# Kernel optimization log

Measured on AMD Instinct MI355X. Metric: run time of the kernel, lower is better.

## Reference

```python
import jax, jax.numpy as jnp
import numpy as np

NUM_ITERS = 5
MIN_SCALE = 0.5
MAX_SCALE = 2.0
EPS = 1e-8


def setup_inputs() -> dict:
    key = jax.random.key(0)
    k1, k2 = jax.random.split(key)
    B, N, M = 16, 4096, 4096
    source = jax.random.normal(k1, (B, N, 3), dtype=jnp.float32)
    target = jax.random.normal(k2, (B, M, 3), dtype=jnp.float32)
    return {"source": source, "target": target}


def _sq_cdist(a, b):
    # squared euclidean distance matrix (B,N,M) via quadratic expansion
    a2 = jnp.sum(a * a, axis=-1)[:, :, None]
    b2 = jnp.sum(b * b, axis=-1)[:, None, :]
    ab = jnp.einsum('bnd,bmd->bnm', a, b)
    return jnp.maximum(a2 + b2 - 2.0 * ab, 0.0)


def _umeyama(source, target_corr):
    # optimal similarity transform (R, t, scale), Umeyama
    B = source.shape[0]
    mu_src = jnp.mean(source, axis=1, keepdims=True)       # (B,1,3)
    mu_tgt = jnp.mean(target_corr, axis=1, keepdims=True)  # (B,1,3)
    src_c = source - mu_src
    tgt_c = target_corr - mu_tgt
    H = jnp.einsum('bnd,bne->bde', src_c, tgt_c)           # (B,3,3)
    U, S, Vh = jnp.linalg.svd(H)
    V = jnp.swapaxes(Vh, 1, 2)
    det_UV = jnp.linalg.det(jnp.einsum('bij,bkj->bik', V, U))  # det(V U^T)
    d_diag = jnp.concatenate(
        [jnp.ones((B, 2), dtype=source.dtype), det_UV[:, None]], axis=1)  # (B,3)
    # R = V @ diag(d) @ U^T
    R = jnp.einsum('bij,bj,bkj->bik', V, d_diag, U)
    var_src = jnp.sum(src_c * src_c, axis=(1, 2))          # (B,)
    trace_S = jnp.sum(S * d_diag, axis=1)                  # (B,)
    scale = (trace_S / (var_src + EPS))[:, None, None]
    scale = jnp.clip(scale, MIN_SCALE, MAX_SCALE)
    t = mu_tgt - scale * jnp.einsum('bnd,bed->bne', mu_src, R)
    return R, t, scale


def reference(source, target):
    # ICP iterations (no-grad in original -> stop_gradient on final transform)
    src_current = source
    for _ in range(NUM_ITERS):
        dist = _sq_cdist(src_current, target)              # (B,N,M)
        min_idx = jnp.argmin(dist, axis=2)                 # (B,N)
        tgt_corr = jnp.take_along_axis(target, min_idx[:, :, None], axis=1)
        R, t, scale = _umeyama(source, tgt_corr)
        src_current = scale * jnp.einsum('bnd,bed->bne', source, R) + t
    R = jax.lax.stop_gradient(R)
    t = jax.lax.stop_gradient(t)
    scale = jax.lax.stop_gradient(scale)
    aligned_source = scale * jnp.einsum('bnd,bed->bne', source, R) + t
    final_dist = _sq_cdist(aligned_source, target)
    min_src2tgt = jnp.min(final_dist, axis=2)
    min_tgt2src = jnp.min(final_dist, axis=1)
    chamfer = jnp.mean(min_src2tgt, axis=1) + jnp.mean(min_tgt2src, axis=1)
    return jnp.mean(chamfer), aligned_source
```

## Files before the change

kernel.cpp:

```cpp
#include <hip/hip_runtime.h>
#include <math.h>

#define BLOCK 256
#define NB    16
#define NN_   4096
#define MM_   4096
#define NITER 5
#define P     4
#define SCH   4
#define KCH   32
#define TCH   128
#define KCHF  16
#define TCHF  256
#define B2    1024

#define OFF_STATS 0
#define OFF_T     64
#define OFF_CH    320
#define OFF_ND    2048
#define OFF_FA    67584
#define OFF_FB    133120
#define CLR_BASE  2048
#define CLR_CNT   196608

typedef __attribute__((ext_vector_type(2))) float f32x2;

__device__ __forceinline__ f32x2 pk_fma(f32x2 a, f32x2 b, f32x2 c) {
#if defined(__has_builtin) && __has_builtin(__builtin_elementwise_fma)
  return __builtin_elementwise_fma(a, b, c);
#else
  return a * b + c;
#endif
}

__device__ __forceinline__ void atomic_min_f(float* p, float v) {
  atomicMin((unsigned int*)p, __float_as_uint(v));
}

__global__ __launch_bounds__(BLOCK) void icp_init(const float* __restrict__ src,
                                                  float* __restrict__ ws) {
  int b = blockIdx.x, tid = threadIdx.x;
  for (int i = b*BLOCK + tid; i < CLR_CNT; i += NB*BLOCK)
    ws[CLR_BASE + i] = INFINITY;
  const float* sb = src + (size_t)b * NN_ * 3;
  float sx = 0.f, sy = 0.f, sz = 0.f, ss = 0.f;
  for (int n = tid; n < NN_; n += BLOCK) {
    float x = sb[3*n], y = sb[3*n+1], z = sb[3*n+2];
    sx += x; sy += y; sz += z;
    ss += fmaf(x, x, fmaf(y, y, z*z));
  }
  __shared__ float red[16];
  for (int m = 32; m; m >>= 1) {
    sx += __shfl_xor(sx, m); sy += __shfl_xor(sy, m);
    sz += __shfl_xor(sz, m); ss += __shfl_xor(ss, m);
  }
  int wave = tid >> 6;
  if ((tid & 63) == 0) {
    red[wave*4+0] = sx; red[wave*4+1] = sy; red[wave*4+2] = sz; red[wave*4+3] = ss;
  }
  __syncthreads();
  if (tid == 0) {
    for (int w = 1; w < 4; ++w) {
      sx += red[w*4+0]; sy += red[w*4+1]; sz += red[w*4+2]; ss += red[w*4+3];
    }
    float* st = ws + OFF_STATS + b*4;
    st[0] = sx; st[1] = sy; st[2] = sz; st[3] = ss;
    float* T = ws + OFF_T + b*16;
    T[0]=1.f; T[1]=0.f; T[2]=0.f;
    T[3]=0.f; T[4]=1.f; T[5]=0.f;
    T[6]=0.f; T[7]=0.f; T[8]=1.f;
    T[9]=0.f; T[10]=0.f; T[11]=0.f; T[12]=1.f;
  }
}

__global__ __launch_bounds__(BLOCK, 8) void icp_nn1(const float* __restrict__ src,
                                                    const float* __restrict__ tgt,
                                                    float* __restrict__ ws) {
  __shared__ __align__(16) float tx_[TCH], ty_[TCH], tz_[TCH], tw_[TCH];
  int b = blockIdx.z, kc = blockIdx.y, tid = threadIdx.x;
  int n0 = blockIdx.x * (BLOCK * P) + tid;
  const float* T = ws + OFF_T + b*16;
  float sc = T[12];
  f32x2 nxp[P], nyp[P], nzp[P], p2p[P];
#pragma unroll
  for (int k = 0; k < P; ++k) {
    const float* sp = src + ((size_t)b * NN_ + n0 + k*BLOCK) * 3;
    float sx = sp[0], sy = sp[1], sz = sp[2];
    float px = fmaf(sc, fmaf(T[0], sx, fmaf(T[1], sy, T[2]*sz)), T[9]);
    float py = fmaf(sc, fmaf(T[3], sx, fmaf(T[4], sy, T[5]*sz)), T[10]);
    float pz = fmaf(sc, fmaf(T[6], sx, fmaf(T[7], sy, T[8]*sz)), T[11]);
    nxp[k].x = nxp[k].y = -2.f*px;
    nyp[k].x = nyp[k].y = -2.f*py;
    nzp[k].x = nzp[k].y = -2.f*pz;
    float p2 = fmaf(px, px, fmaf(py, py, pz*pz));
    p2p[k].x = p2p[k].y = p2;
  }
  if (tid < TCH) {
    int j = tid;
    const float* tp = tgt + ((size_t)b * MM_ + kc * TCH + j) * 3;
    float tx = tp[0], ty = tp[1], tz = tp[2];
    tx_[j] = tx; ty_[j] = ty; tz_[j] = tz;
    tw_[j] = fmaf(tx, tx, fmaf(ty, ty, tz*tz));
  }
  __syncthreads();

  int jbase = kc * TCH;
  float best[P];
#pragma unroll
  for (int k = 0; k < P; ++k) best[k] = INFINITY;
#pragma unroll 4
  for (int j = 0; j < TCH; j += 2) {
    f32x2 TX = *(const f32x2*)&tx_[j];
    f32x2 TY = *(const f32x2*)&ty_[j];
    f32x2 TZ = *(const f32x2*)&tz_[j];
    f32x2 TW = *(const f32x2*)&tw_[j];
    unsigned i0 = (unsigned)(jbase + j), i1 = i0 + 1;
#pragma unroll
    for (int k = 0; k < P; ++k) {
      f32x2 v = pk_fma(nxp[k], TX, pk_fma(nyp[k], TY, pk_fma(nzp[k], TZ, TW + p2p[k])));
      float p0 = __uint_as_float((__float_as_uint(v.x) & 0xFFFFF000u) | i0);
      float p1 = __uint_as_float((__float_as_uint(v.y) & 0xFFFFF000u) | i1);
      best[k] = fminf(fminf(p0, p1), best[k]);
    }
  }
#pragma unroll
  for (int k = 0; k < P; ++k)
    atomic_min_f(ws + OFF_ND + (size_t)b*NN_ + n0 + k*BLOCK, best[k]);
}

__global__ __launch_bounds__(B2) void icp_nn2u(const float* __restrict__ src,
                                               const float* __restrict__ tgt,
                                               float* __restrict__ ws) {
  __shared__ float red[16*12];
  __shared__ float sums[12];
  int b = blockIdx.x, tid = threadIdx.x;
  float acc[12];
#pragma unroll
  for (int c = 0; c < 12; ++c) acc[c] = 0.f;
  for (int g = 0; g < NN_/B2; ++g) {
    int n = g*B2 + tid;
    size_t slot = OFF_ND + (size_t)b*NN_ + n;
    float bd = ws[slot];
    ws[slot] = INFINITY;
    int bi = (int)(__float_as_uint(bd) & 4095u);
    const float* tp = tgt + ((size_t)b * MM_ + bi) * 3;
    const float* sp = src + ((size_t)b * NN_ + n) * 3;
    float tx = tp[0], ty = tp[1], tz = tp[2];
    float sx = sp[0], sy = sp[1], sz = sp[2];
    acc[0] += tx; acc[1] += ty; acc[2] += tz;
    acc[3] += sx*tx; acc[4] += sx*ty; acc[5] += sx*tz;
    acc[6] += sy*tx; acc[7] += sy*ty; acc[8] += sy*tz;
    acc[9] += sz*tx; acc[10] += sz*ty; acc[11] += sz*tz;
  }
#pragma unroll
  for (int c = 0; c < 12; ++c)
    for (int m = 32; m; m >>= 1) acc[c] += __shfl_xor(acc[c], m);
  int wave = tid >> 6;
  if ((tid & 63) == 0) {
#pragma unroll
    for (int c = 0; c < 12; ++c) red[wave*12 + c] = acc[c];
  }
  __syncthreads();
  if (tid < 12) {
    float s = 0.f;
    for (int w = 0; w < 16; ++w) s += red[w*12 + tid];
    sums[tid] = s;
  }
  __syncthreads();
  if (tid != 0) return;

  const float* st = ws + OFF_STATS + b*4;
  const float N = (float)NN_;
  float mus[3] = {st[0]/N, st[1]/N, st[2]/N};
  float var_src = st[3] - N*(mus[0]*mus[0] + mus[1]*mus[1] + mus[2]*mus[2]);
  float mut[3] = {sums[0]/N, sums[1]/N, sums[2]/N};
  float H[3][3];
  for (int d = 0; d < 3; ++d)
    for (int e = 0; e < 3; ++e)
      H[d][e] = sums[3 + 3*d + e] - N*mus[d]*mut[e];

  float A[3][3];
  for (int i = 0; i < 3; ++i)
    for (int j = 0; j < 3; ++j)
      A[i][j] = H[0][i]*H[0][j] + H[1][i]*H[1][j] + H[2][i]*H[2][j];
  float V[3][3] = {{1,0,0},{0,1,0},{0,0,1}};
  const int PP[3] = {0,0,1}, QQ[3] = {1,2,2};
  for (int sweep = 0; sweep < 7; ++sweep) {
    for (int r = 0; r < 3; ++r) {
      int p = PP[r], q = QQ[r];
      float apq = A[p][q];
      if (fabsf(apq) < 1e-30f) continue;
      float tau = (A[q][q] - A[p][p]) / (2.f*apq);
      float tt = (tau >= 0.f ? 1.f : -1.f) / (fabsf(tau) + sqrtf(1.f + tau*tau));
      float c = rsqrtf(1.f + tt*tt), s = tt*c;
      for (int k = 0; k < 3; ++k) { float akp=A[k][p], akq=A[k][q];
        A[k][p]=c*akp - s*akq; A[k][q]=s*akp + c*akq; }
      for (int k = 0; k < 3; ++k) { float apk=A[p][k], aqk=A[q][k];
        A[p][k]=c*apk - s*aqk; A[q][k]=s*apk + c*aqk; }
      for (int k = 0; k < 3; ++k) { float vkp=V[k][p], vkq=V[k][q];
        V[k][p]=c*vkp - s*vkq; V[k][q]=s*vkp + c*vkq; }
    }
  }
  float lam[3] = {A[0][0], A[1][1], A[2][2]};
  int o[3] = {0,1,2};
  if (lam[o[1]] > lam[o[0]]) { int t_=o[0]; o[0]=o[1]; o[1]=t_; }
  if (lam[o[2]] > lam[o[0]]) { int t_=o[0]; o[0]=o[2]; o[2]=t_; }
  if (lam[o[2]] > lam[o[1]]) { int t_=o[1]; o[1]=o[2]; o[2]=t_; }
  float v0[3] = {V[0][o[0]], V[1][o[0]], V[2][o[0]]};
  float v1[3] = {V[0][o[1]], V[1][o[1]], V[2][o[1]]};
  float v2[3] = {V[0][o[2]], V[1][o[2]], V[2][o[2]]};

  float hv0[3], hv1[3], hv2[3];
  for (int d = 0; d < 3; ++d) {
    hv0[d] = H[d][0]*v0[0] + H[d][1]*v0[1] + H[d][2]*v0[2];
    hv1[d] = H[d][0]*v1[0] + H[d][1]*v1[1] + H[d][2]*v1[2];
    hv2[d] = H[d][0]*v2[0] + H[d][1]*v2[1] + H[d][2]*v2[2];
  }
  float S0 = sqrtf(hv0[0]*hv0[0] + hv0[1]*hv0[1] + hv0[2]*hv0[2]);
  float u0[3];
  float inv0 = (S0 > 1e-20f) ? 1.f/S0 : 0.f;
  u0[0]=hv0[0]*inv0; u0[1]=hv0[1]*inv0; u0[2]=hv0[2]*inv0;
  if (S0 <= 1e-20f) { u0[0]=1.f; u0[1]=0.f; u0[2]=0.f; }
  float S1 = sqrtf(hv1[0]*hv1[0] + hv1[1]*hv1[1] + hv1[2]*hv1[2]);
  float d01 = u0[0]*hv1[0] + u0[1]*hv1[1] + u0[2]*hv1[2];
  float w1[3] = {hv1[0]-d01*u0[0], hv1[1]-d01*u0[1], hv1[2]-d01*u0[2]};
  float n1 = sqrtf(w1[0]*w1[0] + w1[1]*w1[1] + w1[2]*w1[2]);
  float u1[3];
  if (n1 > 1e-20f) { u1[0]=w1[0]/n1; u1[1]=w1[1]/n1; u1[2]=w1[2]/n1; }
  else {
    float ax = fabsf(u0[0]);
    float t0[3] = { ax < 0.9f ? 1.f : 0.f, ax < 0.9f ? 0.f : 1.f, 0.f };
    u1[0] = u0[1]*t0[2]-u0[2]*t0[1];
    u1[1] = u0[2]*t0[0]-u0[0]*t0[2];
    u1[2] = u0[0]*t0[1]-u0[1]*t0[0];
    float nn = sqrtf(u1[0]*u1[0]+u1[1]*u1[1]+u1[2]*u1[2]);
    u1[0]/=nn; u1[1]/=nn; u1[2]/=nn;
  }
  float u2[3] = {u0[1]*u1[2]-u0[2]*u1[1],
                 u0[2]*u1[0]-u0[0]*u1[2],
                 u0[0]*u1[1]-u0[1]*u1[0]};
  float s2p = u2[0]*hv2[0] + u2[1]*hv2[1] + u2[2]*hv2[2];
  float dV = v0[0]*(v1[1]*v2[2]-v1[2]*v2[1])
           - v0[1]*(v1[0]*v2[2]-v1[2]*v2[0])
           + v0[2]*(v1[0]*v2[1]-v1[1]*v2[0]);
  dV = (dV >= 0.f) ? 1.f : -1.f;
  float traceS = S0 + S1 + dV * s2p;

  float R[3][3];
  for (int i = 0; i < 3; ++i)
    for (int k = 0; k < 3; ++k)
      R[i][k] = v0[i]*u0[k] + v1[i]*u1[k] + dV*v2[i]*u2[k];

  float scale = traceS / (var_src + 1e-8f);
  scale = fminf(fmaxf(scale, 0.5f), 2.0f);
  float tv[3];
  for (int e = 0; e < 3; ++e)
    tv[e] = mut[e] - scale*(R[e][0]*mus[0] + R[e][1]*mus[1] + R[e][2]*mus[2]);

  float* T = ws + OFF_T + b*16;
  for (int e = 0; e < 3; ++e)
    for (int d = 0; d < 3; ++d)
      T[3*e + d] = R[e][d];
  T[9]  = tv[0]; T[10] = tv[1]; T[11] = tv[2];
  T[12] = scale;
}

__global__ __launch_bounds__(BLOCK, 8) void icp_final(const float* __restrict__ src,
                                                      const float* __restrict__ tgt,
                                                      float* __restrict__ out,
                                                      float* __restrict__ ws) {
  __shared__ __align__(16) float tx_[TCHF], ty_[TCHF], tz_[TCHF], tw_[TCHF];
  int b = blockIdx.z, yk = blockIdx.y, tid = threadIdx.x;
  int dir = yk >> 4, kc = yk & 15;
  const float* T = ws + OFF_T + b*16;
  float sc = T[12];
  int n0 = blockIdx.x * (BLOCK * P) + tid;
  f32x2 nxp[P], nyp[P], nzp[P];
  float pp[P];

  if (dir == 0) {
#pragma unroll
    for (int k = 0; k < P; ++k) {
      const float* sp = src + ((size_t)b * NN_ + n0 + k*BLOCK) * 3;
      float sx = sp[0], sy = sp[1], sz = sp[2];
      float px = fmaf(sc, fmaf(T[0], sx, fmaf(T[1], sy, T[2]*sz)), T[9]);
      float py = fmaf(sc, fmaf(T[3], sx, fmaf(T[4], sy, T[5]*sz)), T[10]);
      float pz = fmaf(sc, fmaf(T[6], sx, fmaf(T[7], sy, T[8]*sz)), T[11]);
      if (kc == 0) {
        float* op = out + 1 + ((size_t)b * NN_ + n0 + k*BLOCK) * 3;
        op[0] = px; op[1] = py; op[2] = pz;
      }
      pp[k] = fmaf(px, px, fmaf(py, py, pz*pz));
      nxp[k].x = nxp[k].y = -2.f*px;
      nyp[k].x = nyp[k].y = -2.f*py;
      nzp[k].x = nzp[k].y = -2.f*pz;
    }
    const float* tb = tgt + ((size_t)b * MM_ + kc * TCHF) * 3;
    {
      int j = tid;
      float tx = tb[3*j], ty = tb[3*j+1], tz = tb[3*j+2];
      tx_[j] = tx; ty_[j] = ty; tz_[j] = tz;
      tw_[j] = fmaf(tx, tx, fmaf(ty, ty, tz*tz));
    }
  } else {
#pragma unroll
    for (int k = 0; k < P; ++k) {
      const float* qp = tgt + ((size_t)b * MM_ + n0 + k*BLOCK) * 3;
      float qx = qp[0], qy = qp[1], qz = qp[2];
      pp[k] = fmaf(qx, qx, fmaf(qy, qy, qz*qz));
      nxp[k].x = nxp[k].y = -2.f*qx;
      nyp[k].x = nyp[k].y = -2.f*qy;
      nzp[k].x = nzp[k].y = -2.f*qz;
    }
    const float* sb = src + ((size_t)b * NN_ + kc * TCHF) * 3;
    {
      int j = tid;
      float sx = sb[3*j], sy = sb[3*j+1], sz = sb[3*j+2];
      float ax = fmaf(sc, fmaf(T[0], sx, fmaf(T[1], sy, T[2]*sz)), T[9]);
      float ay = fmaf(sc, fmaf(T[3], sx, fmaf(T[4], sy, T[5]*sz)), T[10]);
      float az = fmaf(sc, fmaf(T[6], sx, fmaf(T[7], sy, T[8]*sz)), T[11]);
      tx_[j] = ax; ty_[j] = ay; tz_[j] = az;
      tw_[j] = fmaf(ax, ax, fmaf(ay, ay, az*az));
    }
  }
  __syncthreads();

  float best[P];
#pragma unroll
  for (int k = 0; k < P; ++k) best[k] = INFINITY;
#pragma unroll 4
  for (int j = 0; j < TCHF; j += 2) {
    f32x2 TX = *(const f32x2*)&tx_[j];
    f32x2 TY = *(const f32x2*)&ty_[j];
    f32x2 TZ = *(const f32x2*)&tz_[j];
    f32x2 TW = *(const f32x2*)&tw_[j];
#pragma unroll
    for (int k = 0; k < P; ++k) {
      f32x2 v = pk_fma(nxp[k], TX, pk_fma(nyp[k], TY, pk_fma(nzp[k], TZ, TW)));
      best[k] = fminf(fminf(v.x, v.y), best[k]);
    }
  }
  float* dst = ws + (dir ? OFF_FB : OFF_FA);
#pragma unroll
  for (int k = 0; k < P; ++k) {
    float v = fmaxf(best[k] + pp[k], 0.f);
    atomic_min_f(dst + (size_t)b*NN_ + n0 + k*BLOCK, v);
  }
}

__global__ __launch_bounds__(BLOCK) void icp_fcomb(float* __restrict__ ws) {
  __shared__ float red[4*2];
  int b = blockIdx.x, tid = threadIdx.x;
  float sa = 0.f, sb = 0.f;
  for (int g = 0; g < NN_/BLOCK; ++g) {
    int n = g*BLOCK + tid;
    sa += ws[OFF_FA + (size_t)b*NN_ + n];
    sb += ws[OFF_FB + (size_t)b*NN_ + n];
  }
  for (int m = 32; m; m >>= 1) {
    sa += __shfl_xor(sa, m); sb += __shfl_xor(sb, m);
  }
  int wave = tid >> 6;
  if ((tid & 63) == 0) { red[wave*2] = sa; red[wave*2+1] = sb; }
  __syncthreads();
  if (tid == 0) {
    sa = red[0] + red[2] + red[4] + red[6];
    sb = red[1] + red[3] + red[5] + red[7];
    ws[OFF_CH + b] = sa / (float)NN_ + sb / (float)MM_;
  }
}

__global__ __launch_bounds__(64) void icp_finalize(float* __restrict__ out,
                                                   const float* __restrict__ ws) {
  if (threadIdx.x == 0) {
    float s = 0.f;
    for (int b = 0; b < NB; ++b) s += ws[OFF_CH + b];
    out[0] = s / (float)NB;
  }
}

extern "C" void kernel_launch(void* const* d_in, const int* in_sizes, int n_in,
                              void* d_out, int out_size, void* d_ws, size_t ws_size,
                              hipStream_t stream) {
  const float* src = (const float*)d_in[0];
  const float* tgt = (const float*)d_in[1];
  float* out = (float*)d_out;
  float* ws  = (float*)d_ws;

  icp_init<<<NB, BLOCK, 0, stream>>>(src, ws);
  for (int it = 0; it < NITER; ++it) {
    icp_nn1<<<dim3(SCH, KCH, NB), BLOCK, 0, stream>>>(src, tgt, ws);
    icp_nn2u<<<NB, B2, 0, stream>>>(src, tgt, ws);
  }
  icp_final<<<dim3(SCH, 2*KCHF, NB), BLOCK, 0, stream>>>(src, tgt, out, ws);
  icp_fcomb<<<NB, BLOCK, 0, stream>>>(ws);
  icp_finalize<<<1, 64, 0, stream>>>(out, ws);
}
```

Measured before the change: 304.8 us.

## Fuse Umeyama update and chamfer reduction into last-block tails via atomic counters

Removes the separate icp_nn2u, icp_fcomb and icp_finalize launches. Each per-batch reduction now runs in whichever block of the preceding nearest-neighbour kernel finishes last, detected with a threadfence plus an atomic counter. This cuts kernel launches from 14 to 7 and the launch gaps between them. In exchange, the correspondence gather and SVD run on 256 threads instead of 1024, serialising on one block per batch, and the reads and resets go through atomics.

```diff
diff --git a/kernel.cpp b/kernel.cpp
--- a/kernel.cpp
+++ b/kernel.cpp
@@ -12,11 +12,13 @@
 #define TCH   128
 #define KCHF  16
 #define TCHF  256
-#define B2    1024
 
 #define OFF_STATS 0
 #define OFF_T     64
 #define OFF_CH    320
+#define OFF_CNT   1024
+#define OFF_CNTF  1040
+#define OFF_CNTG  1056
 #define OFF_ND    2048
 #define OFF_FA    67584
 #define OFF_FB    133120
@@ -36,12 +38,20 @@
 __device__ __forceinline__ void atomic_min_f(float* p, float v) {
   atomicMin((unsigned int*)p, __float_as_uint(v));
 }
+__device__ __forceinline__ float atomic_ld_f(float* p) {
+  return __uint_as_float(atomicAdd((unsigned int*)p, 0u));
+}
+__device__ __forceinline__ void atomic_st_f(float* p, float v) {
+  atomicExch((unsigned int*)p, __float_as_uint(v));
+}
 
 __global__ __launch_bounds__(BLOCK) void icp_init(const float* __restrict__ src,
                                                   float* __restrict__ ws) {
   int b = blockIdx.x, tid = threadIdx.x;
   for (int i = b*BLOCK + tid; i < CLR_CNT; i += NB*BLOCK)
     ws[CLR_BASE + i] = INFINITY;
+  if (b == 0 && tid < 64)
+    ((unsigned*)(ws + OFF_CNT))[tid] = 0u;
   const float* sb = src + (size_t)b * NN_ * 3;
   float sx = 0.f, sy = 0.f, sz = 0.f, ss = 0.f;
   for (int n = tid; n < NN_; n += BLOCK) {
@@ -77,71 +87,79 @@
                                                     const float* __restrict__ tgt,
                                                     float* __restrict__ ws) {
   __shared__ __align__(16) float tx_[TCH], ty_[TCH], tz_[TCH], tw_[TCH];
+  __shared__ float redA[4*12];
+  __shared__ float sums[12];
+  __shared__ int lastFlag;
   int b = blockIdx.z, kc = blockIdx.y, tid = threadIdx.x;
   int n0 = blockIdx.x * (BLOCK * P) + tid;
-  const float* T = ws + OFF_T + b*16;
-  float sc = T[12];
-  f32x2 nxp[P], nyp[P], nzp[P], p2p[P];
-#pragma unroll
-  for (int k = 0; k < P; ++k) {
-    const float* sp = src + ((size_t)b * NN_ + n0 + k*BLOCK) * 3;
-    float sx = sp[0], sy = sp[1], sz = sp[2];
-    float px = fmaf(sc, fmaf(T[0], sx, fmaf(T[1], sy, T[2]*sz)), T[9]);
-    float py = fmaf(sc, fmaf(T[3], sx, fmaf(T[4], sy, T[5]*sz)), T[10]);
-    float pz = fmaf(sc, fmaf(T[6], sx, fmaf(T[7], sy, T[8]*sz)), T[11]);
-    nxp[k].x = nxp[k].y = -2.f*px;
-    nyp[k].x = nyp[k].y = -2.f*py;
-    nzp[k].x = nzp[k].y = -2.f*pz;
-    float p2 = fmaf(px, px, fmaf(py, py, pz*pz));
-    p2p[k].x = p2p[k].y = p2;
-  }
-  if (tid < TCH) {
-    int j = tid;
-    const float* tp = tgt + ((size_t)b * MM_ + kc * TCH + j) * 3;
-    float tx = tp[0], ty = tp[1], tz = tp[2];
-    tx_[j] = tx; ty_[j] = ty; tz_[j] = tz;
-    tw_[j] = fmaf(tx, tx, fmaf(ty, ty, tz*tz));
-  }
-  __syncthreads();
-
-  int jbase = kc * TCH;
-  float best[P];
-#pragma unroll
-  for (int k = 0; k < P; ++k) best[k] = INFINITY;
+  {
+    const float* T = ws + OFF_T + b*16;
+    float sc = T[12];
+    f32x2 nxp[P], nyp[P], nzp[P], p2p[P];
+#pragma unroll
+    for (int k = 0; k < P; ++k) {
+      const float* sp = src + ((size_t)b * NN_ + n0 + k*BLOCK) * 3;
+      float sx = sp[0], sy = sp[1], sz = sp[2];
+      float px = fmaf(sc, fmaf(T[0], sx, fmaf(T[1], sy, T[2]*sz)), T[9]);
+      float py = fmaf(sc, fmaf(T[3], sx, fmaf(T[4], sy, T[5]*sz)), T[10]);
+      float pz = fmaf(sc, fmaf(T[6], sx, fmaf(T[7], sy, T[8]*sz)), T[11]);
+      nxp[k].x = nxp[k].y = -2.f*px;
+      nyp[k].x = nyp[k].y = -2.f*py;
+      nzp[k].x = nzp[k].y = -2.f*pz;
+      float p2 = fmaf(px, px, fmaf(py, py, pz*pz));
+      p2p[k].x = p2p[k].y = p2;
+    }
+    if (tid < TCH) {
+      int j = tid;
+      const float* tp = tgt + ((size_t)b * MM_ + kc * TCH + j) * 3;
+      float tx = tp[0], ty = tp[1], tz = tp[2];
+      tx_[j] = tx; ty_[j] = ty; tz_[j] = tz;
+      tw_[j] = fmaf(tx, tx, fmaf(ty, ty, tz*tz));
+    }
+    __syncthreads();
+
+    int jbase = kc * TCH;
+    float best[P];
+#pragma unroll
+    for (int k = 0; k < P; ++k) best[k] = INFINITY;
 #pragma unroll 4
-  for (int j = 0; j < TCH; j += 2) {
-    f32x2 TX = *(const f32x2*)&tx_[j];
-    f32x2 TY = *(const f32x2*)&ty_[j];
-    f32x2 TZ = *(const f32x2*)&tz_[j];
-    f32x2 TW = *(const f32x2*)&tw_[j];
-    unsigned i0 = (unsigned)(jbase + j), i1 = i0 + 1;
-#pragma unroll
-    for (int k = 0; k < P; ++k) {
-      f32x2 v = pk_fma(nxp[k], TX, pk_fma(nyp[k], TY, pk_fma(nzp[k], TZ, TW + p2p[k])));
-      float p0 = __uint_as_float((__float_as_uint(v.x) & 0xFFFFF000u) | i0);
-      float p1 = __uint_as_float((__float_as_uint(v.y) & 0xFFFFF000u) | i1);
-      best[k] = fminf(fminf(p0, p1), best[k]);
-    }
-  }
-#pragma unroll
-  for (int k = 0; k < P; ++k)
-    atomic_min_f(ws + OFF_ND + (size_t)b*NN_ + n0 + k*BLOCK, best[k]);
-}
-
-__global__ __launch_bounds__(B2) void icp_nn2u(const float* __restrict__ src,
-                                               const float* __restrict__ tgt,
-                                               float* __restrict__ ws) {
-  __shared__ float red[16*12];
-  __shared__ float sums[12];
-  int b = blockIdx.x, tid = threadIdx.x;
+    for (int j = 0; j < TCH; j += 2) {
+      f32x2 TX = *(const f32x2*)&tx_[j];
+      f32x2 TY = *(const f32x2*)&ty_[j];
+      f32x2 TZ = *(const f32x2*)&tz_[j];
+      f32x2 TW = *(const f32x2*)&tw_[j];
+      unsigned i0 = (unsigned)(jbase + j), i1 = i0 + 1;
+#pragma unroll
+      for (int k = 0; k < P; ++k) {
+        f32x2 v = pk_fma(nxp[k], TX, pk_fma(nyp[k], TY, pk_fma(nzp[k], TZ, TW + p2p[k])));
+        float p0 = __uint_as_float((__float_as_uint(v.x) & 0xFFFFF000u) | i0);
+        float p1 = __uint_as_float((__float_as_uint(v.y) & 0xFFFFF000u) | i1);
+        best[k] = fminf(fminf(p0, p1), best[k]);
+      }
+    }
+#pragma unroll
+    for (int k = 0; k < P; ++k)
+      atomic_min_f(ws + OFF_ND + (size_t)b*NN_ + n0 + k*BLOCK, best[k]);
+  }
+
+  __syncthreads();
+  if (tid == 0) {
+    __threadfence();
+    unsigned d = atomicAdd((unsigned*)(ws + OFF_CNT) + b, 1u);
+    lastFlag = (d == (unsigned)(SCH*KCH - 1));
+    if (lastFlag) atomicExch((unsigned*)(ws + OFF_CNT) + b, 0u);
+  }
+  __syncthreads();
+  if (!lastFlag) return;
+
   float acc[12];
 #pragma unroll
   for (int c = 0; c < 12; ++c) acc[c] = 0.f;
-  for (int g = 0; g < NN_/B2; ++g) {
-    int n = g*B2 + tid;
-    size_t slot = OFF_ND + (size_t)b*NN_ + n;
-    float bd = ws[slot];
-    ws[slot] = INFINITY;
+  for (int g = 0; g < NN_/BLOCK; ++g) {
+    int n = g*BLOCK + tid;
+    float* slot = ws + OFF_ND + (size_t)b*NN_ + n;
+    float bd = atomic_ld_f(slot);
+    atomic_st_f(slot, INFINITY);
     int bi = (int)(__float_as_uint(bd) & 4095u);
     const float* tp = tgt + ((size_t)b * MM_ + bi) * 3;
     const float* sp = src + ((size_t)b * NN_ + n) * 3;
@@ -158,14 +176,11 @@
   int wave = tid >> 6;
   if ((tid & 63) == 0) {
 #pragma unroll
-    for (int c = 0; c < 12; ++c) red[wave*12 + c] = acc[c];
-  }
-  __syncthreads();
-  if (tid < 12) {
-    float s = 0.f;
-    for (int w = 0; w < 16; ++w) s += red[w*12 + tid];
-    sums[tid] = s;
-  }
+    for (int c = 0; c < 12; ++c) redA[wave*12 + c] = acc[c];
+  }
+  __syncthreads();
+  if (tid < 12)
+    sums[tid] = redA[tid] + redA[12+tid] + redA[24+tid] + redA[36+tid];
   __syncthreads();
   if (tid != 0) return;
 
@@ -270,111 +285,121 @@
                                                       float* __restrict__ out,
                                                       float* __restrict__ ws) {
   __shared__ __align__(16) float tx_[TCHF], ty_[TCHF], tz_[TCHF], tw_[TCHF];
+  __shared__ float red8[8];
+  __shared__ int lastFlag, lastG;
   int b = blockIdx.z, yk = blockIdx.y, tid = threadIdx.x;
   int dir = yk >> 4, kc = yk & 15;
-  const float* T = ws + OFF_T + b*16;
-  float sc = T[12];
-  int n0 = blockIdx.x * (BLOCK * P) + tid;
-  f32x2 nxp[P], nyp[P], nzp[P];
-  float pp[P];
-
-  if (dir == 0) {
+  {
+    const float* T = ws + OFF_T + b*16;
+    float sc = T[12];
+    int n0 = blockIdx.x * (BLOCK * P) + tid;
+    f32x2 nxp[P], nyp[P], nzp[P];
+    float pp[P];
+
+    if (dir == 0) {
+#pragma unroll
+      for (int k = 0; k < P; ++k) {
+        const float* sp = src + ((size_t)b * NN_ + n0 + k*BLOCK) * 3;
+        float sx = sp[0], sy = sp[1], sz = sp[2];
+        float px = fmaf(sc, fmaf(T[0], sx, fmaf(T[1], sy, T[2]*sz)), T[9]);
+        float py = fmaf(sc, fmaf(T[3], sx, fmaf(T[4], sy, T[5]*sz)), T[10]);
+        float pz = fmaf(sc, fmaf(T[6], sx, fmaf(T[7], sy, T[8]*sz)), T[11]);
+        if (kc == 0) {
+          float* op = out + 1 + ((size_t)b * NN_ + n0 + k*BLOCK) * 3;
+          op[0] = px; op[1] = py; op[2] = pz;
+        }
+        pp[k] = fmaf(px, px, fmaf(py, py, pz*pz));
+        nxp[k].x = nxp[k].y = -2.f*px;
+        nyp[k].x = nyp[k].y = -2.f*py;
+        nzp[k].x = nzp[k].y = -2.f*pz;
+      }
+      const float* tb = tgt + ((size_t)b * MM_ + kc * TCHF) * 3;
+      {
+        int j = tid;
+        float tx = tb[3*j], ty = tb[3*j+1], tz = tb[3*j+2];
+        tx_[j] = tx; ty_[j] = ty; tz_[j] = tz;
+        tw_[j] = fmaf(tx, tx, fmaf(ty, ty, tz*tz));
+      }
+    } else {
+#pragma unroll
+      for (int k = 0; k < P; ++k) {
+        const float* qp = tgt + ((size_t)b * MM_ + n0 + k*BLOCK) * 3;
+        float qx = qp[0], qy = qp[1], qz = qp[2];
+        pp[k] = fmaf(qx, qx, fmaf(qy, qy, qz*qz));
+        nxp[k].x = nxp[k].y = -2.f*qx;
+        nyp[k].x = nyp[k].y = -2.f*qy;
+        nzp[k].x = nzp[k].y = -2.f*qz;
+      }
+      const float* sb = src + ((size_t)b * NN_ + kc * TCHF) * 3;
+      {
+        int j = tid;
+        float sx = sb[3*j], sy = sb[3*j+1], sz = sb[3*j+2];
+        float ax = fmaf(sc, fmaf(T[0], sx, fmaf(T[1], sy, T[2]*sz)), T[9]);
+        float ay = fmaf(sc, fmaf(T[3], sx, fmaf(T[4], sy, T[5]*sz)), T[10]);
+        float az = fmaf(sc, fmaf(T[6], sx, fmaf(T[7], sy, T[8]*sz)), T[11]);
+        tx_[j] = ax; ty_[j] = ay; tz_[j] = az;
+        tw_[j] = fmaf(ax, ax, fmaf(ay, ay, az*az));
+      }
+    }
+    __syncthreads();
+
+    float best[P];
+#pragma unroll
+    for (int k = 0; k < P; ++k) best[k] = INFINITY;
+#pragma unroll 4
+    for (int j = 0; j < TCHF; j += 2) {
+      f32x2 TX = *(const f32x2*)&tx_[j];
+      f32x2 TY = *(const f32x2*)&ty_[j];
+      f32x2 TZ = *(const f32x2*)&tz_[j];
+      f32x2 TW = *(const f32x2*)&tw_[j];
+#pragma unroll
+      for (int k = 0; k < P; ++k) {
+        f32x2 v = pk_fma(nxp[k], TX, pk_fma(nyp[k], TY, pk_fma(nzp[k], TZ, TW)));
+        best[k] = fminf(fminf(v.x, v.y), best[k]);
+      }
+    }
+    float* dst = ws + (dir ? OFF_FB : OFF_FA);
 #pragma unroll
     for (int k = 0; k < P; ++k) {
-      const float* sp = src + ((size_t)b * NN_ + n0 + k*BLOCK) * 3;
-      float sx = sp[0], sy = sp[1], sz = sp[2];
-      float px = fmaf(sc, fmaf(T[0], sx, fmaf(T[1], sy, T[2]*sz)), T[9]);
-      float py = fmaf(sc, fmaf(T[3], sx, fmaf(T[4], sy, T[5]*sz)), T[10]);
-      float pz = fmaf(sc, fmaf(T[6], sx, fmaf(T[7], sy, T[8]*sz)), T[11]);
-      if (kc == 0) {
-        float* op = out + 1 + ((size_t)b * NN_ + n0 + k*BLOCK) * 3;
-        op[0] = px; op[1] = py; op[2] = pz;
-      }
-      pp[k] = fmaf(px, px, fmaf(py, py, pz*pz));
-      nxp[k].x = nxp[k].y = -2.f*px;
-      nyp[k].x = nyp[k].y = -2.f*py;
-      nzp[k].x = nzp[k].y = -2.f*pz;
-    }
-    const float* tb = tgt + ((size_t)b * MM_ + kc * TCHF) * 3;
-    {
-      int j = tid;
-      float tx = tb[3*j], ty = tb[3*j+1], tz = tb[3*j+2];
-      tx_[j] = tx; ty_[j] = ty; tz_[j] = tz;
-      tw_[j] = fmaf(tx, tx, fmaf(ty, ty, tz*tz));
-    }
-  } else {
-#pragma unroll
-    for (int k = 0; k < P; ++k) {
-      const float* qp = tgt + ((size_t)b * MM_ + n0 + k*BLOCK) * 3;
-      float qx = qp[0], qy = qp[1], qz = qp[2];
-      pp[k] = fmaf(qx, qx, fmaf(qy, qy, qz*qz));
-      nxp[k].x = nxp[k].y = -2.f*qx;
-      nyp[k].x = nyp[k].y = -2.f*qy;
-      nzp[k].x = nzp[k].y = -2.f*qz;
-    }
-    const float* sb = src + ((size_t)b * NN_ + kc * TCHF) * 3;
-    {
-      int j = tid;
-      float sx = sb[3*j], sy = sb[3*j+1], sz = sb[3*j+2];
-      float ax = fmaf(sc, fmaf(T[0], sx, fmaf(T[1], sy, T[2]*sz)), T[9]);
-      float ay = fmaf(sc, fmaf(T[3], sx, fmaf(T[4], sy, T[5]*sz)), T[10]);
-      float az = fmaf(sc, fmaf(T[6], sx, fmaf(T[7], sy, T[8]*sz)), T[11]);
-      tx_[j] = ax; ty_[j] = ay; tz_[j] = az;
-      tw_[j] = fmaf(ax, ax, fmaf(ay, ay, az*az));
-    }
-  }
-  __syncthreads();
-
-  float best[P];
-#pragma unroll
-  for (int k = 0; k < P; ++k) best[k] = INFINITY;
-#pragma unroll 4
-  for (int j = 0; j < TCHF; j += 2) {
-    f32x2 TX = *(const f32x2*)&tx_[j];
-    f32x2 TY = *(const f32x2*)&ty_[j];
-    f32x2 TZ = *(const f32x2*)&tz_[j];
-    f32x2 TW = *(const f32x2*)&tw_[j];
-#pragma unroll
-    for (int k = 0; k < P; ++k) {
-      f32x2 v = pk_fma(nxp[k], TX, pk_fma(nyp[k], TY, pk_fma(nzp[k], TZ, TW)));
-      best[k] = fminf(fminf(v.x, v.y), best[k]);
-    }
-  }
-  float* dst = ws + (dir ? OFF_FB : OFF_FA);
-#pragma unroll
-  for (int k = 0; k < P; ++k) {
-    float v = fmaxf(best[k] + pp[k], 0.f);
-    atomic_min_f(dst + (size_t)b*NN_ + n0 + k*BLOCK, v);
-  }
-}
-
-__global__ __launch_bounds__(BLOCK) void icp_fcomb(float* __restrict__ ws) {
-  __shared__ float red[4*2];
-  int b = blockIdx.x, tid = threadIdx.x;
-  float sa = 0.f, sb = 0.f;
+      float v = fmaxf(best[k] + pp[k], 0.f);
+      atomic_min_f(dst + (size_t)b*NN_ + n0 + k*BLOCK, v);
+    }
+  }
+
+  __syncthreads();
+  if (tid == 0) {
+    __threadfence();
+    unsigned d = atomicAdd((unsigned*)(ws + OFF_CNTF) + b, 1u);
+    lastFlag = (d == (unsigned)(SCH*2*KCHF - 1));
+    if (lastFlag) atomicExch((unsigned*)(ws + OFF_CNTF) + b, 0u);
+  }
+  __syncthreads();
+  if (!lastFlag) return;
+
+  float sa = 0.f, sb2 = 0.f;
   for (int g = 0; g < NN_/BLOCK; ++g) {
     int n = g*BLOCK + tid;
-    sa += ws[OFF_FA + (size_t)b*NN_ + n];
-    sb += ws[OFF_FB + (size_t)b*NN_ + n];
+    sa  += atomic_ld_f(ws + OFF_FA + (size_t)b*NN_ + n);
+    sb2 += atomic_ld_f(ws + OFF_FB + (size_t)b*NN_ + n);
   }
   for (int m = 32; m; m >>= 1) {
-    sa += __shfl_xor(sa, m); sb += __shfl_xor(sb, m);
+    sa += __shfl_xor(sa, m); sb2 += __shfl_xor(sb2, m);
   }
   int wave = tid >> 6;
-  if ((tid & 63) == 0) { red[wave*2] = sa; red[wave*2+1] = sb; }
+  if ((tid & 63) == 0) { red8[wave*2] = sa; red8[wave*2+1] = sb2; }
   __syncthreads();
   if (tid == 0) {
-    sa = red[0] + red[2] + red[4] + red[6];
-    sb = red[1] + red[3] + red[5] + red[7];
-    ws[OFF_CH + b] = sa / (float)NN_ + sb / (float)MM_;
-  }
-}
-
-__global__ __launch_bounds__(64) void icp_finalize(float* __restrict__ out,
-                                                   const float* __restrict__ ws) {
-  if (threadIdx.x == 0) {
+    sa  = red8[0] + red8[2] + red8[4] + red8[6];
+    sb2 = red8[1] + red8[3] + red8[5] + red8[7];
+    atomic_st_f(ws + OFF_CH + b, sa / (float)NN_ + sb2 / (float)MM_);
+    unsigned g = atomicAdd((unsigned*)(ws + OFF_CNTG), 1u);
+    lastG = (g == (unsigned)(NB - 1));
+    if (lastG) atomicExch((unsigned*)(ws + OFF_CNTG), 0u);
+  }
+  __syncthreads();
+  if (lastG && tid == 0) {
     float s = 0.f;
-    for (int b = 0; b < NB; ++b) s += ws[OFF_CH + b];
+    for (int bb = 0; bb < NB; ++bb) s += atomic_ld_f(ws + OFF_CH + bb);
     out[0] = s / (float)NB;
   }
 }
@@ -388,11 +413,7 @@
   float* ws  = (float*)d_ws;
 
   icp_init<<<NB, BLOCK, 0, stream>>>(src, ws);
-  for (int it = 0; it < NITER; ++it) {
+  for (int it = 0; it < NITER; ++it)
     icp_nn1<<<dim3(SCH, KCH, NB), BLOCK, 0, stream>>>(src, tgt, ws);
-    icp_nn2u<<<NB, B2, 0, stream>>>(src, tgt, ws);
-  }
   icp_final<<<dim3(SCH, 2*KCHF, NB), BLOCK, 0, stream>>>(src, tgt, out, ws);
-  icp_fcomb<<<NB, BLOCK, 0, stream>>>(ws);
-  icp_finalize<<<1, 64, 0, stream>>>(out, ws);
-}
+}
```

Measured after the change: 597.6 us. 1.96x slower.
